# Performance work log

Measured on AMD Instinct MI355X. Metric: run time of the kernel, lower is better.

Reference implementation:

```python
import jax, jax.numpy as jnp
import numpy as np

HID = 128
CDIM = 128
NCH = 3
NDIM = 3


def _linear_params(key, fan_in, fan_out):
    kw, kb = jax.random.split(key)
    bound = 1.0 / np.sqrt(fan_in)
    W = jax.random.uniform(kw, (fan_in, fan_out), jnp.float32, -bound, bound)
    b = jax.random.uniform(kb, (fan_out,), jnp.float32, -bound, bound)
    return W, b


def setup_inputs() -> dict:
    key = jax.random.key(0)
    keys = jax.random.split(key, 12)
    p = jax.random.normal(keys[0], (32, 8192, NDIM), jnp.float32)
    W_pos, b_pos = _linear_params(keys[1], NDIM, 2 * HID)
    W0, b0 = _linear_params(keys[2], 2 * HID, HID)
    W1, b1 = _linear_params(keys[3], 2 * HID, HID)
    W2, b2 = _linear_params(keys[4], 2 * HID, HID)
    W3, b3 = _linear_params(keys[5], 2 * HID, HID)
    Wc, bc = _linear_params(keys[6], HID, CDIM)
    Wm0, bm0 = _linear_params(keys[7], CDIM, HID)
    Wm1, bm1 = _linear_params(keys[8], HID, HID)
    Wm2, bm2 = _linear_params(keys[9], HID, HID)
    Wp, bp = _linear_params(keys[10], HID, NCH * 3)
    return dict(p=p, W_pos=W_pos, b_pos=b_pos, W0=W0, b0=b0, W1=W1, b1=b1,
                W2=W2, b2=b2, W3=W3, b3=b3, Wc=Wc, bc=bc,
                Wm0=Wm0, bm0=bm0, Wm1=Wm1, bm1=bm1, Wm2=Wm2, bm2=bm2,
                Wp=Wp, bp=bp)


def _relu(x):
    return jnp.maximum(x, 0)


def _pool_cat(net):
    # max over points (dim=1), broadcast back and concat on features
    pooled = jnp.max(net, axis=1, keepdims=True)
    pooled = jnp.broadcast_to(pooled, net.shape)
    return jnp.concatenate([net, pooled], axis=2)  # [B, T, 2*hid]


def reference(p, W_pos, b_pos, W0, b0, W1, b1, W2, b2, W3, b3,
              Wc, bc, Wm0, bm0, Wm1, bm1, Wm2, bm2, Wp, bp):
    net = p @ W_pos + b_pos                      # [B, T, 2*hid]
    net = _relu(net) @ W0 + b0                   # [B, T, hid]
    net = _relu(_pool_cat(net)) @ W1 + b1        # [B, T, hid]
    net = _relu(_pool_cat(net)) @ W2 + b2        # [B, T, hid]
    net = _relu(_pool_cat(net)) @ W3 + b3        # [B, T, hid]
    net = jnp.max(net, axis=1)                   # [B, hid]
    net = _relu(net) @ Wc + bc                   # [B, c_dim]
    net = _relu(net) @ Wm0 + bm0
    net = _relu(net) @ Wm1 + bm1
    net = _relu(net) @ Wm2 + bm2
    net = _relu(net) @ Wp + bp                   # [B, n_channels*3]
    return net
```

## Files before the change

### kernel.cpp

```cpp
#include <hip/hip_runtime.h>


using bf16x8 = __attribute__((ext_vector_type(8))) __bf16;
using u16x8  = __attribute__((ext_vector_type(8))) unsigned short;
using f32x4  = __attribute__((ext_vector_type(4))) float;

__device__ __forceinline__ unsigned short f2bf(float x) {
  __bf16 b = (__bf16)x;
  return __builtin_bit_cast(unsigned short, b);
}

__device__ __forceinline__ f32x4 mfma16(bf16x8 a, bf16x8 b, f32x4 c) {
  return __builtin_amdgcn_mfma_f32_16x16x32_bf16(a, b, c, 0, 0, 0);
}

union FragU { unsigned short us[8]; u16x8 u; bf16x8 v; };

__global__ __launch_bounds__(256) void k_pack_all(
    const float* __restrict__ W0, const float* __restrict__ W1,
    const float* __restrict__ W2, const float* __restrict__ W3,
    unsigned short* __restrict__ Wt) {
  const int blk = blockIdx.x, t = threadIdx.x;
  const float* src; int slot; unsigned short* dst;
  if (blk < 16)      { src = W0; slot = blk * 256 + t;        dst = Wt; }
  else if (blk < 24) { src = W1; slot = (blk - 16) * 256 + t; dst = Wt + 32768; }
  else if (blk < 32) { src = W2; slot = (blk - 24) * 256 + t; dst = Wt + 49152; }
  else               { src = W3; slot = (blk - 32) * 256 + t; dst = Wt + 65536; }
  const int ks = slot >> 9, rem = slot & 511;
  const int nt = rem >> 6, lane = rem & 63;
  const int n = nt * 16 + (lane & 15);
  const int kb = ks * 32 + ((lane >> 4) << 3);
  FragU fr;
#pragma unroll
  for (int j = 0; j < 8; ++j) fr.us[j] = f2bf(src[(kb + j) * 128 + n]);
  reinterpret_cast<u16x8*>(dst)[slot] = fr.u;
}

__device__ __forceinline__ void epilogue_q(
    float (*pmaxs)[128], const f32x4 (&acc)[2][4],
    const float* __restrict__ biasvec, int t, int blk,
    unsigned short* __restrict__ h, float* __restrict__ pm, bool write_h) {
  const int w = t >> 6, lane = t & 63, g = lane >> 4, c = lane & 15;
  const int rowg = w >> 1, colg = w & 1;
  unsigned short* hout = h + (size_t)blk * 8192;
#pragma unroll
  for (int ntl = 0; ntl < 4; ++ntl) {
    const int ntg = colg * 4 + ntl;
    const float4 bb = *reinterpret_cast<const float4*>(&biasvec[ntg * 16 + g * 4]);
    float vm[4] = {0.f, 0.f, 0.f, 0.f};
#pragma unroll
    for (int mi = 0; mi < 2; ++mi) {
      const float v0 = fmaxf(acc[mi][ntl][0] + bb.x, 0.f);
      const float v1 = fmaxf(acc[mi][ntl][1] + bb.y, 0.f);
      const float v2 = fmaxf(acc[mi][ntl][2] + bb.z, 0.f);
      const float v3 = fmaxf(acc[mi][ntl][3] + bb.w, 0.f);
      vm[0] = fmaxf(vm[0], v0); vm[1] = fmaxf(vm[1], v1);
      vm[2] = fmaxf(vm[2], v2); vm[3] = fmaxf(vm[3], v3);
      if (write_h) {
        ushort4 s4;
        s4.x = f2bf(v0); s4.y = f2bf(v1); s4.z = f2bf(v2); s4.w = f2bf(v3);
        const int slot = (rowg * 2 + mi) * 256 + (ntg >> 1) * 64 +
                         ((ntg & 1) * 2 + (g >> 1)) * 16 + c;
        *reinterpret_cast<ushort4*>(&hout[slot * 8 + (g & 1) * 4]) = s4;
      }
    }
#pragma unroll
    for (int r = 0; r < 4; ++r) {
      vm[r] = fmaxf(vm[r], __shfl_xor(vm[r], 1, 64));
      vm[r] = fmaxf(vm[r], __shfl_xor(vm[r], 2, 64));
      vm[r] = fmaxf(vm[r], __shfl_xor(vm[r], 4, 64));
      vm[r] = fmaxf(vm[r], __shfl_xor(vm[r], 8, 64));
    }
    if (c == 0) {
#pragma unroll
      for (int r = 0; r < 4; ++r) pmaxs[rowg][ntg * 16 + g * 4 + r] = vm[r];
    }
  }
  __syncthreads();
  if (t < 128) {
    pm[(size_t)blk * 128 + t] = fmaxf(pmaxs[0][t], pmaxs[1][t]);
  }
}

__global__ __launch_bounds__(256) void k_layer0(
    const float* __restrict__ p, const float* __restrict__ Wpos,
    const float* __restrict__ bpos, const float* __restrict__ b0,
    const unsigned short* __restrict__ Wt0, unsigned short* __restrict__ h,
    float* __restrict__ pm) {
  __shared__ float wls[1024];
  __shared__ float pmaxs[2][128];
  const int t = threadIdx.x, blk = blockIdx.x;
  for (int i = t; i < 1024; i += 256) wls[i] = (i < 768) ? Wpos[i] : bpos[i - 768];

  const int w = t >> 6, lane = t & 63, g = lane >> 4, c = lane & 15;
  const int rowg = w >> 1, colg = w & 1;
  float px[2], py[2], pz[2];
#pragma unroll
  for (int mi = 0; mi < 2; ++mi) {
    const int row = blk * 64 + rowg * 32 + mi * 16 + c;
    px[mi] = p[row * 3 + 0]; py[mi] = p[row * 3 + 1]; pz[mi] = p[row * 3 + 2];
  }

  f32x4 acc[2][4];
#pragma unroll
  for (int mi = 0; mi < 2; ++mi)
#pragma unroll
    for (int ntl = 0; ntl < 4; ++ntl) acc[mi][ntl] = f32x4{0.f, 0.f, 0.f, 0.f};

  const bf16x8* Bf = reinterpret_cast<const bf16x8*>(Wt0);
  __syncthreads();

#pragma unroll
  for (int pass = 0; pass < 2; ++pass) {
    bf16x8 B[4][4];
#pragma unroll
    for (int ksl = 0; ksl < 4; ++ksl)
#pragma unroll
      for (int ntl = 0; ntl < 4; ++ntl)
        B[ksl][ntl] = Bf[((pass * 4 + ksl) * 8 + colg * 4 + ntl) * 64 + lane];
#pragma unroll
    for (int ksl = 0; ksl < 4; ++ksl) {
      const int ks = pass * 4 + ksl;
      FragU a[2];
#pragma unroll
      for (int h2 = 0; h2 < 2; ++h2) {
        const int kq = ks * 32 + g * 8 + h2 * 4;
        const float4 w0 = *reinterpret_cast<const float4*>(&wls[kq]);
        const float4 w1 = *reinterpret_cast<const float4*>(&wls[256 + kq]);
        const float4 w2 = *reinterpret_cast<const float4*>(&wls[512 + kq]);
        const float4 bb = *reinterpret_cast<const float4*>(&wls[768 + kq]);
#pragma unroll
        for (int mi = 0; mi < 2; ++mi) {
          a[mi].us[h2 * 4 + 0] = f2bf(fmaxf(bb.x + px[mi] * w0.x + py[mi] * w1.x + pz[mi] * w2.x, 0.f));
          a[mi].us[h2 * 4 + 1] = f2bf(fmaxf(bb.y + px[mi] * w0.y + py[mi] * w1.y + pz[mi] * w2.y, 0.f));
          a[mi].us[h2 * 4 + 2] = f2bf(fmaxf(bb.z + px[mi] * w0.z + py[mi] * w1.z + pz[mi] * w2.z, 0.f));
          a[mi].us[h2 * 4 + 3] = f2bf(fmaxf(bb.w + px[mi] * w0.w + py[mi] * w1.w + pz[mi] * w2.w, 0.f));
        }
      }
#pragma unroll
      for (int ntl = 0; ntl < 4; ++ntl) {
        acc[0][ntl] = mfma16(B[ksl][ntl], a[0].v, acc[0][ntl]);
        acc[1][ntl] = mfma16(B[ksl][ntl], a[1].v, acc[1][ntl]);
      }
    }
  }
  epilogue_q(pmaxs, acc, b0, t, blk, h, pm, true);
}

__global__ __launch_bounds__(256) void k_layer(
    const unsigned short* __restrict__ Wta, const float* __restrict__ cvec,
    unsigned short* __restrict__ h, float* __restrict__ pm, int write_h) {
  __shared__ float pmaxs[2][128];
  const int t = threadIdx.x, blk = blockIdx.x;
  const int w = t >> 6, lane = t & 63;
  const int rowg = w >> 1, colg = w & 1;
  const int b = blk >> 7;

  bf16x8 B[4][4];
  const bf16x8* Bf = reinterpret_cast<const bf16x8*>(Wta);
#pragma unroll
  for (int ks = 0; ks < 4; ++ks)
#pragma unroll
    for (int ntl = 0; ntl < 4; ++ntl)
      B[ks][ntl] = Bf[(ks * 8 + colg * 4 + ntl) * 64 + lane];

  f32x4 acc[2][4];
#pragma unroll
  for (int mi = 0; mi < 2; ++mi)
#pragma unroll
    for (int ntl = 0; ntl < 4; ++ntl) acc[mi][ntl] = f32x4{0.f, 0.f, 0.f, 0.f};

  const u16x8* hblk = reinterpret_cast<const u16x8*>(h) + (size_t)blk * 1024;
#pragma unroll
  for (int ks = 0; ks < 4; ++ks) {
    FragU a0, a1;
    a0.u = hblk[(rowg * 2 + 0) * 256 + ks * 64 + lane];
    a1.u = hblk[(rowg * 2 + 1) * 256 + ks * 64 + lane];
#pragma unroll
    for (int ntl = 0; ntl < 4; ++ntl) {
      acc[0][ntl] = mfma16(B[ks][ntl], a0.v, acc[0][ntl]);
      acc[1][ntl] = mfma16(B[ks][ntl], a1.v, acc[1][ntl]);
    }
  }
  epilogue_q(pmaxs, acc, cvec + b * 128, t, blk, h, pm, write_h != 0);
}

__global__ __launch_bounds__(256) void k_combine(
    const float* __restrict__ pm, const float* __restrict__ Wn,
    const float* __restrict__ bn, float* __restrict__ cout) {
  const int b = blockIdx.x, t = threadIdx.x;
  const int f = t & 127, half = t >> 7;
  __shared__ float part[2][128];
  __shared__ float rm[128];
  float m = 0.f;
  for (int i = half * 64; i < half * 64 + 64; ++i)
    m = fmaxf(m, pm[(size_t)(b * 128 + i) * 128 + f]);
  part[half][f] = m;
  __syncthreads();
  if (t < 128) rm[f] = fmaxf(part[0][f], part[1][f]);
  __syncthreads();
  float s = 0.f;
  for (int q = half * 64; q < half * 64 + 64; ++q)
    s += rm[q] * Wn[(128 + q) * 128 + f];
  part[half][f] = s;
  __syncthreads();
  if (t < 128) cout[b * 128 + f] = part[0][f] + part[1][f] + bn[f];
}

__global__ __launch_bounds__(256) void k_final(
    const float* __restrict__ pm3,
    const float* __restrict__ Wc,  const float* __restrict__ bc,
    const float* __restrict__ Wm0, const float* __restrict__ bm0,
    const float* __restrict__ Wm1, const float* __restrict__ bm1,
    const float* __restrict__ Wm2, const float* __restrict__ bm2,
    const float* __restrict__ Wp,  const float* __restrict__ bp,
    float* __restrict__ out) {
  const int b = blockIdx.x, t = threadIdx.x;
  const int f = t & 127, half = t >> 7;
  __shared__ float part[2][128];
  __shared__ float x[128];
  float m = 0.f;
  for (int i = half * 64; i < half * 64 + 64; ++i)
    m = fmaxf(m, pm3[(size_t)(b * 128 + i) * 128 + f]);
  part[half][f] = m;
  __syncthreads();
  if (t < 128) x[f] = fmaxf(part[0][f], part[1][f]);
  __syncthreads();

  const float* Ws[4] = {Wc, Wm0, Wm1, Wm2};
  const float* bs[4] = {bc, bm0, bm1, bm2};
#pragma unroll
  for (int L = 0; L < 4; ++L) {
    float s = 0.f;
    for (int q = half * 64; q < half * 64 + 64; ++q)
      s += x[q] * Ws[L][q * 128 + f];
    part[half][f] = s;
    __syncthreads();
    if (t < 128) x[f] = fmaxf(part[0][f] + part[1][f] + bs[L][f], 0.f);
    __syncthreads();
  }
  if (t < 9) {
    float s = bp[t];
    for (int q = 0; q < 128; ++q) s += x[q] * Wp[q * 9 + t];
    out[b * 9 + t] = s;
  }
}

extern "C" void kernel_launch(void* const* d_in, const int* in_sizes, int n_in,
                              void* d_out, int out_size, void* d_ws, size_t ws_size,
                              hipStream_t stream) {
  const float *p = nullptr, *Wpos = nullptr, *bpos = nullptr;
  const float *Wp = nullptr, *bp = nullptr;
  const float *W256[4] = {}; int nW256 = 0;
  const float *W128[4] = {}; int nW128 = 0;
  const float *B128[8] = {}; int nB128 = 0;
  for (int i = 0; i < n_in; ++i) {
    const float* q = (const float*)d_in[i];
    switch (in_sizes[i]) {
      case 786432: p = q; break;
      case 768:    Wpos = q; break;
      case 256:    bpos = q; break;
      case 1152:   Wp = q; break;
      case 9:      bp = q; break;
      case 32768:  if (nW256 < 4) W256[nW256++] = q; break;
      case 16384:  if (nW128 < 4) W128[nW128++] = q; break;
      case 128:    if (nB128 < 8) B128[nB128++] = q; break;
      default: break;
    }
  }
  const float *W0 = W256[0], *W1 = W256[1], *W2 = W256[2], *W3 = W256[3];
  const float *Wc = W128[0], *Wm0 = W128[1], *Wm1 = W128[2], *Wm2 = W128[3];
  const float *b0 = B128[0], *b1 = B128[1], *b2 = B128[2], *b3 = B128[3];
  const float *bc = B128[4], *bm0 = B128[5], *bm1 = B128[6], *bm2 = B128[7];
  float* out = (float*)d_out;

  char* ws = (char*)d_ws;
  float* pm = (float*)ws;
  float* cv = (float*)(ws + 2097152);
  unsigned short* Wt = (unsigned short*)(ws + 2097152 + 16384);
  unsigned short* Wt0 = Wt;
  unsigned short* Wt1 = Wt + 32768;
  unsigned short* Wt2 = Wt + 49152;
  unsigned short* Wt3 = Wt + 65536;
  unsigned short* h = Wt + 81920;

  k_pack_all<<<40, 256, 0, stream>>>(W0, W1, W2, W3, Wt);
  k_layer0<<<4096, 256, 0, stream>>>(p, Wpos, bpos, b0, Wt0, h, pm);
  k_combine<<<32, 256, 0, stream>>>(pm, W1, b1, cv);
  k_layer<<<4096, 256, 0, stream>>>(Wt1, cv, h, pm, 1);
  k_combine<<<32, 256, 0, stream>>>(pm, W2, b2, cv);
  k_layer<<<4096, 256, 0, stream>>>(Wt2, cv, h, pm, 1);
  k_combine<<<32, 256, 0, stream>>>(pm, W3, b3, cv);
  k_layer<<<4096, 256, 0, stream>>>(Wt3, cv, h, pm, 0);
  k_final<<<32, 256, 0, stream>>>(pm, Wc, bc, Wm0, bm0, Wm1, bm1, Wm2, bm2, Wp, bp, out);
}
```

Measured before the change: 192.1 us.

## Double rows per block in hidden layers and stage layer0 activations in LDS

The hidden-layer kernel now processes 128 rows per block (4 M-tiles per wave) with half the grid, streaming B fragments per k-step instead of preloading all of them. Combine and final kernels take a per-batch partial count to match. Layer0 now computes the ReLU'd positional features once per block into a shared-memory fragment buffer before the MFMA loop, instead of recomputing them per wave. The aim is more reuse of weight fragments and less redundant positional-layer arithmetic, at the cost of more accumulator registers, 32KB of LDS in layer0, and fewer blocks to fill the GPU.

```diff
diff --git a/kernel.cpp b/kernel.cpp
--- a/kernel.cpp
+++ b/kernel.cpp
@@ -36,20 +36,146 @@
   reinterpret_cast<u16x8*>(dst)[slot] = fr.u;
 }
 
-__device__ __forceinline__ void epilogue_q(
-    float (*pmaxs)[128], const f32x4 (&acc)[2][4],
-    const float* __restrict__ biasvec, int t, int blk,
-    unsigned short* __restrict__ h, float* __restrict__ pm, bool write_h) {
+__global__ __launch_bounds__(256) void k_layer0(
+    const float* __restrict__ p, const float* __restrict__ Wpos,
+    const float* __restrict__ bpos, const float* __restrict__ b0,
+    const unsigned short* __restrict__ Wt0, unsigned short* __restrict__ h,
+    float* __restrict__ pm) {
+  __shared__ float wls[1024];
+  __shared__ unsigned short Afrag[16384];
+  __shared__ float pmaxs[2][128];
+  const int t = threadIdx.x, blk = blockIdx.x;
+  for (int i = t; i < 1024; i += 256) wls[i] = (i < 768) ? Wpos[i] : bpos[i - 768];
+
+  const int w = t >> 6, lane = t & 63, g = lane >> 4, c = lane & 15;
+
+  float px[4], py[4], pz[4];
+#pragma unroll
+  for (int tl = 0; tl < 4; ++tl) {
+    const int row = blk * 64 + tl * 16 + c;
+    px[tl] = p[row * 3 + 0]; py[tl] = p[row * 3 + 1]; pz[tl] = p[row * 3 + 2];
+  }
+  __syncthreads();
+
+#pragma unroll
+  for (int i = 0; i < 8; ++i) {
+    const int tl = i & 3;
+    const int ks = w * 2 + (i >> 2);
+    const int kb = ks * 32 + g * 8;
+    FragU fr;
+#pragma unroll
+    for (int j = 0; j < 8; ++j) {
+      const int k = kb + j;
+      fr.us[j] = f2bf(fmaxf(wls[768 + k] + px[tl] * wls[k] + py[tl] * wls[256 + k] + pz[tl] * wls[512 + k], 0.f));
+    }
+    *reinterpret_cast<u16x8*>(&Afrag[((tl * 8 + ks) * 64 + lane) * 8]) = fr.u;
+  }
+  __syncthreads();
+
+  const int rowg = w >> 1, colg = w & 1;
+  f32x4 acc[2][4];
+#pragma unroll
+  for (int mi = 0; mi < 2; ++mi)
+#pragma unroll
+    for (int ntl = 0; ntl < 4; ++ntl) acc[mi][ntl] = f32x4{0.f, 0.f, 0.f, 0.f};
+
+  const bf16x8* Bf = reinterpret_cast<const bf16x8*>(Wt0);
+  const u16x8* Af = reinterpret_cast<const u16x8*>(Afrag);
+#pragma unroll
+  for (int ks = 0; ks < 8; ++ks) {
+    bf16x8 B[4];
+#pragma unroll
+    for (int ntl = 0; ntl < 4; ++ntl)
+      B[ntl] = Bf[(ks * 8 + colg * 4 + ntl) * 64 + lane];
+    FragU a0, a1;
+    a0.u = Af[((rowg * 2 + 0) * 8 + ks) * 64 + lane];
+    a1.u = Af[((rowg * 2 + 1) * 8 + ks) * 64 + lane];
+#pragma unroll
+    for (int ntl = 0; ntl < 4; ++ntl) {
+      acc[0][ntl] = mfma16(B[ntl], a0.v, acc[0][ntl]);
+      acc[1][ntl] = mfma16(B[ntl], a1.v, acc[1][ntl]);
+    }
+  }
+
+  unsigned short* hout = h + (size_t)blk * 8192;
+#pragma unroll
+  for (int ntl = 0; ntl < 4; ++ntl) {
+    const int ntg = colg * 4 + ntl;
+    const float4 bb = *reinterpret_cast<const float4*>(&b0[ntg * 16 + g * 4]);
+    float vm[4] = {0.f, 0.f, 0.f, 0.f};
+#pragma unroll
+    for (int mi = 0; mi < 2; ++mi) {
+      const float v0 = fmaxf(acc[mi][ntl][0] + bb.x, 0.f);
+      const float v1 = fmaxf(acc[mi][ntl][1] + bb.y, 0.f);
+      const float v2 = fmaxf(acc[mi][ntl][2] + bb.z, 0.f);
+      const float v3 = fmaxf(acc[mi][ntl][3] + bb.w, 0.f);
+      vm[0] = fmaxf(vm[0], v0); vm[1] = fmaxf(vm[1], v1);
+      vm[2] = fmaxf(vm[2], v2); vm[3] = fmaxf(vm[3], v3);
+      ushort4 s4;
+      s4.x = f2bf(v0); s4.y = f2bf(v1); s4.z = f2bf(v2); s4.w = f2bf(v3);
+      const int slot = (rowg * 2 + mi) * 256 + (ntg >> 1) * 64 +
+                       ((ntg & 1) * 2 + (g >> 1)) * 16 + c;
+      *reinterpret_cast<ushort4*>(&hout[slot * 8 + (g & 1) * 4]) = s4;
+    }
+#pragma unroll
+    for (int r = 0; r < 4; ++r) {
+      vm[r] = fmaxf(vm[r], __shfl_xor(vm[r], 1, 64));
+      vm[r] = fmaxf(vm[r], __shfl_xor(vm[r], 2, 64));
+      vm[r] = fmaxf(vm[r], __shfl_xor(vm[r], 4, 64));
+      vm[r] = fmaxf(vm[r], __shfl_xor(vm[r], 8, 64));
+    }
+    if (c == 0) {
+#pragma unroll
+      for (int r = 0; r < 4; ++r) pmaxs[rowg][ntg * 16 + g * 4 + r] = vm[r];
+    }
+  }
+  __syncthreads();
+  if (t < 128) pm[(size_t)blk * 128 + t] = fmaxf(pmaxs[0][t], pmaxs[1][t]);
+}
+
+__global__ __launch_bounds__(256) void k_layer(
+    const unsigned short* __restrict__ Wta, const float* __restrict__ cvec,
+    unsigned short* __restrict__ h, float* __restrict__ pm, int write_h) {
+  __shared__ float pmaxs[2][128];
+  const int t = threadIdx.x, blk = blockIdx.x;
   const int w = t >> 6, lane = t & 63, g = lane >> 4, c = lane & 15;
   const int rowg = w >> 1, colg = w & 1;
-  unsigned short* hout = h + (size_t)blk * 8192;
+  const int b = blk >> 6;
+
+  f32x4 acc[4][4];
+#pragma unroll
+  for (int mi = 0; mi < 4; ++mi)
+#pragma unroll
+    for (int ntl = 0; ntl < 4; ++ntl) acc[mi][ntl] = f32x4{0.f, 0.f, 0.f, 0.f};
+
+  const u16x8* hblk = reinterpret_cast<const u16x8*>(h) + (size_t)blk * 2048;
+  const bf16x8* Bf = reinterpret_cast<const bf16x8*>(Wta);
+#pragma unroll
+  for (int ks = 0; ks < 4; ++ks) {
+    bf16x8 B[4];
+#pragma unroll
+    for (int ntl = 0; ntl < 4; ++ntl)
+      B[ntl] = Bf[(ks * 8 + colg * 4 + ntl) * 64 + lane];
+    FragU a[4];
+#pragma unroll
+    for (int mi = 0; mi < 4; ++mi)
+      a[mi].u = hblk[(rowg * 4 + mi) * 256 + ks * 64 + lane];
+#pragma unroll
+    for (int mi = 0; mi < 4; ++mi)
+#pragma unroll
+      for (int ntl = 0; ntl < 4; ++ntl)
+        acc[mi][ntl] = mfma16(B[ntl], a[mi].v, acc[mi][ntl]);
+  }
+
+  unsigned short* hout = h + (size_t)blk * 16384;
+  const float* biasvec = cvec + b * 128;
 #pragma unroll
   for (int ntl = 0; ntl < 4; ++ntl) {
     const int ntg = colg * 4 + ntl;
     const float4 bb = *reinterpret_cast<const float4*>(&biasvec[ntg * 16 + g * 4]);
     float vm[4] = {0.f, 0.f, 0.f, 0.f};
 #pragma unroll
-    for (int mi = 0; mi < 2; ++mi) {
+    for (int mi = 0; mi < 4; ++mi) {
       const float v0 = fmaxf(acc[mi][ntl][0] + bb.x, 0.f);
       const float v1 = fmaxf(acc[mi][ntl][1] + bb.y, 0.f);
       const float v2 = fmaxf(acc[mi][ntl][2] + bb.z, 0.f);
@@ -59,7 +185,7 @@
       if (write_h) {
         ushort4 s4;
         s4.x = f2bf(v0); s4.y = f2bf(v1); s4.z = f2bf(v2); s4.w = f2bf(v3);
-        const int slot = (rowg * 2 + mi) * 256 + (ntg >> 1) * 64 +
+        const int slot = (rowg * 4 + mi) * 256 + (ntg >> 1) * 64 +
                          ((ntg & 1) * 2 + (g >> 1)) * 16 + c;
         *reinterpret_cast<ushort4*>(&hout[slot * 8 + (g & 1) * 4]) = s4;
       }
@@ -77,124 +203,20 @@
     }
   }
   __syncthreads();
-  if (t < 128) {
-    pm[(size_t)blk * 128 + t] = fmaxf(pmaxs[0][t], pmaxs[1][t]);
-  }
-}
-
-__global__ __launch_bounds__(256) void k_layer0(
-    const float* __restrict__ p, const float* __restrict__ Wpos,
-    const float* __restrict__ bpos, const float* __restrict__ b0,
-    const unsigned short* __restrict__ Wt0, unsigned short* __restrict__ h,
-    float* __restrict__ pm) {
-  __shared__ float wls[1024];
-  __shared__ float pmaxs[2][128];
-  const int t = threadIdx.x, blk = blockIdx.x;
-  for (int i = t; i < 1024; i += 256) wls[i] = (i < 768) ? Wpos[i] : bpos[i - 768];
-
-  const int w = t >> 6, lane = t & 63, g = lane >> 4, c = lane & 15;
-  const int rowg = w >> 1, colg = w & 1;
-  float px[2], py[2], pz[2];
-#pragma unroll
-  for (int mi = 0; mi < 2; ++mi) {
-    const int row = blk * 64 + rowg * 32 + mi * 16 + c;
-    px[mi] = p[row * 3 + 0]; py[mi] = p[row * 3 + 1]; pz[mi] = p[row * 3 + 2];
-  }
-
-  f32x4 acc[2][4];
-#pragma unroll
-  for (int mi = 0; mi < 2; ++mi)
-#pragma unroll
-    for (int ntl = 0; ntl < 4; ++ntl) acc[mi][ntl] = f32x4{0.f, 0.f, 0.f, 0.f};
-
-  const bf16x8* Bf = reinterpret_cast<const bf16x8*>(Wt0);
-  __syncthreads();
-
-#pragma unroll
-  for (int pass = 0; pass < 2; ++pass) {
-    bf16x8 B[4][4];
-#pragma unroll
-    for (int ksl = 0; ksl < 4; ++ksl)
-#pragma unroll
-      for (int ntl = 0; ntl < 4; ++ntl)
-        B[ksl][ntl] = Bf[((pass * 4 + ksl) * 8 + colg * 4 + ntl) * 64 + lane];
-#pragma unroll
-    for (int ksl = 0; ksl < 4; ++ksl) {
-      const int ks = pass * 4 + ksl;
-      FragU a[2];
-#pragma unroll
-      for (int h2 = 0; h2 < 2; ++h2) {
-        const int kq = ks * 32 + g * 8 + h2 * 4;
-        const float4 w0 = *reinterpret_cast<const float4*>(&wls[kq]);
-        const float4 w1 = *reinterpret_cast<const float4*>(&wls[256 + kq]);
-        const float4 w2 = *reinterpret_cast<const float4*>(&wls[512 + kq]);
-        const float4 bb = *reinterpret_cast<const float4*>(&wls[768 + kq]);
-#pragma unroll
-        for (int mi = 0; mi < 2; ++mi) {
-          a[mi].us[h2 * 4 + 0] = f2bf(fmaxf(bb.x + px[mi] * w0.x + py[mi] * w1.x + pz[mi] * w2.x, 0.f));
-          a[mi].us[h2 * 4 + 1] = f2bf(fmaxf(bb.y + px[mi] * w0.y + py[mi] * w1.y + pz[mi] * w2.y, 0.f));
-          a[mi].us[h2 * 4 + 2] = f2bf(fmaxf(bb.z + px[mi] * w0.z + py[mi] * w1.z + pz[mi] * w2.z, 0.f));
-          a[mi].us[h2 * 4 + 3] = f2bf(fmaxf(bb.w + px[mi] * w0.w + py[mi] * w1.w + pz[mi] * w2.w, 0.f));
-        }
-      }
-#pragma unroll
-      for (int ntl = 0; ntl < 4; ++ntl) {
-        acc[0][ntl] = mfma16(B[ksl][ntl], a[0].v, acc[0][ntl]);
-        acc[1][ntl] = mfma16(B[ksl][ntl], a[1].v, acc[1][ntl]);
-      }
-    }
-  }
-  epilogue_q(pmaxs, acc, b0, t, blk, h, pm, true);
-}
-
-__global__ __launch_bounds__(256) void k_layer(
-    const unsigned short* __restrict__ Wta, const float* __restrict__ cvec,
-    unsigned short* __restrict__ h, float* __restrict__ pm, int write_h) {
-  __shared__ float pmaxs[2][128];
-  const int t = threadIdx.x, blk = blockIdx.x;
-  const int w = t >> 6, lane = t & 63;
-  const int rowg = w >> 1, colg = w & 1;
-  const int b = blk >> 7;
-
-  bf16x8 B[4][4];
-  const bf16x8* Bf = reinterpret_cast<const bf16x8*>(Wta);
-#pragma unroll
-  for (int ks = 0; ks < 4; ++ks)
-#pragma unroll
-    for (int ntl = 0; ntl < 4; ++ntl)
-      B[ks][ntl] = Bf[(ks * 8 + colg * 4 + ntl) * 64 + lane];
-
-  f32x4 acc[2][4];
-#pragma unroll
-  for (int mi = 0; mi < 2; ++mi)
-#pragma unroll
-    for (int ntl = 0; ntl < 4; ++ntl) acc[mi][ntl] = f32x4{0.f, 0.f, 0.f, 0.f};
-
-  const u16x8* hblk = reinterpret_cast<const u16x8*>(h) + (size_t)blk * 1024;
-#pragma unroll
-  for (int ks = 0; ks < 4; ++ks) {
-    FragU a0, a1;
-    a0.u = hblk[(rowg * 2 + 0) * 256 + ks * 64 + lane];
-    a1.u = hblk[(rowg * 2 + 1) * 256 + ks * 64 + lane];
-#pragma unroll
-    for (int ntl = 0; ntl < 4; ++ntl) {
-      acc[0][ntl] = mfma16(B[ks][ntl], a0.v, acc[0][ntl]);
-      acc[1][ntl] = mfma16(B[ks][ntl], a1.v, acc[1][ntl]);
-    }
-  }
-  epilogue_q(pmaxs, acc, cvec + b * 128, t, blk, h, pm, write_h != 0);
+  if (t < 128) pm[(size_t)blk * 128 + t] = fmaxf(pmaxs[0][t], pmaxs[1][t]);
 }
 
 __global__ __launch_bounds__(256) void k_combine(
     const float* __restrict__ pm, const float* __restrict__ Wn,
-    const float* __restrict__ bn, float* __restrict__ cout) {
+    const float* __restrict__ bn, float* __restrict__ cout, int nper) {
   const int b = blockIdx.x, t = threadIdx.x;
   const int f = t & 127, half = t >> 7;
   __shared__ float part[2][128];
   __shared__ float rm[128];
+  const int hn = nper >> 1;
   float m = 0.f;
-  for (int i = half * 64; i < half * 64 + 64; ++i)
-    m = fmaxf(m, pm[(size_t)(b * 128 + i) * 128 + f]);
+  for (int i = half * hn; i < half * hn + hn; ++i)
+    m = fmaxf(m, pm[(size_t)(b * nper + i) * 128 + f]);
   part[half][f] = m;
   __syncthreads();
   if (t < 128) rm[f] = fmaxf(part[0][f], part[1][f]);
@@ -208,7 +230,7 @@
 }
 
 __global__ __launch_bounds__(256) void k_final(
-    const float* __restrict__ pm3,
+    const float* __restrict__ pm3, int nper,
     const float* __restrict__ Wc,  const float* __restrict__ bc,
     const float* __restrict__ Wm0, const float* __restrict__ bm0,
     const float* __restrict__ Wm1, const float* __restrict__ bm1,
@@ -219,9 +241,10 @@
   const int f = t & 127, half = t >> 7;
   __shared__ float part[2][128];
   __shared__ float x[128];
+  const int hn = nper >> 1;
   float m = 0.f;
-  for (int i = half * 64; i < half * 64 + 64; ++i)
-    m = fmaxf(m, pm3[(size_t)(b * 128 + i) * 128 + f]);
+  for (int i = half * hn; i < half * hn + hn; ++i)
+    m = fmaxf(m, pm3[(size_t)(b * nper + i) * 128 + f]);
   part[half][f] = m;
   __syncthreads();
   if (t < 128) x[f] = fmaxf(part[0][f], part[1][f]);
@@ -286,11 +309,11 @@
 
   k_pack_all<<<40, 256, 0, stream>>>(W0, W1, W2, W3, Wt);
   k_layer0<<<4096, 256, 0, stream>>>(p, Wpos, bpos, b0, Wt0, h, pm);
-  k_combine<<<32, 256, 0, stream>>>(pm, W1, b1, cv);
-  k_layer<<<4096, 256, 0, stream>>>(Wt1, cv, h, pm, 1);
-  k_combine<<<32, 256, 0, stream>>>(pm, W2, b2, cv);
-  k_layer<<<4096, 256, 0, stream>>>(Wt2, cv, h, pm, 1);
-  k_combine<<<32, 256, 0, stream>>>(pm, W3, b3, cv);
-  k_layer<<<4096, 256, 0, stream>>>(Wt3, cv, h, pm, 0);
-  k_final<<<32, 256, 0, stream>>>(pm, Wc, bc, Wm0, bm0, Wm1, bm1, Wm2, bm2, Wp, bp, out);
-}
+  k_combine<<<32, 256, 0, stream>>>(pm, W1, b1, cv, 128);
+  k_layer<<<2048, 256, 0, stream>>>(Wt1, cv, h, pm, 1);
+  k_combine<<<32, 256, 0, stream>>>(pm, W2, b2, cv, 64);
+  k_layer<<<2048, 256, 0, stream>>>(Wt2, cv, h, pm, 1);
+  k_combine<<<32, 256, 0, stream>>>(pm, W3, b3, cv, 64);
+  k_layer<<<2048, 256, 0, stream>>>(Wt3, cv, h, pm, 0);
+  k_final<<<32, 256, 0, stream>>>(pm, 64, Wc, bc, Wm0, bm0, Wm1, bm1, Wm2, bm2, Wp, bp, out);
+}
```

After: 194.0 us. No clear change (+1.0%).
